# Performance work log

Measured on AMD Instinct MI355X. Metric: run time of the kernel, lower is better.

Reference implementation:

```python
import jax, jax.numpy as jnp
import numpy as np
from jax import lax

N_EXPERTS = 16
TOP_K = 2
D_MODEL = 512
D_FF = 2048


def setup_inputs() -> dict:
    key = jax.random.key(0)
    ks = jax.random.split(key, 7)
    s_in = 1.0 / np.sqrt(D_MODEL)
    s_ff = 1.0 / np.sqrt(D_FF)
    x = jax.random.normal(ks[0], (2, 2048, D_MODEL), dtype=jnp.float32)
    router_w = jax.random.uniform(ks[1], (N_EXPERTS, D_MODEL), jnp.float32, -s_in, s_in)
    router_b = jax.random.uniform(ks[2], (N_EXPERTS,), jnp.float32, -s_in, s_in)
    w1 = jax.random.uniform(ks[3], (N_EXPERTS, D_FF, D_MODEL), jnp.float32, -s_in, s_in)
    b1 = jax.random.uniform(ks[4], (N_EXPERTS, D_FF), jnp.float32, -s_in, s_in)
    w2 = jax.random.uniform(ks[5], (N_EXPERTS, D_MODEL, D_FF), jnp.float32, -s_ff, s_ff)
    b2 = jax.random.uniform(ks[6], (N_EXPERTS, D_MODEL), jnp.float32, -s_ff, s_ff)
    return {"x": x, "router_w": router_w, "router_b": router_b,
            "w1": w1, "b1": b1, "w2": w2, "b2": b2}


def reference(x, router_w, router_b, w1, b1, w2, b2):
    B, S, D = x.shape
    xt = x.reshape(-1, D)                                   # [T, D]
    logits = xt @ router_w.T + router_b                     # [T, E]
    probs = jax.nn.softmax(logits, axis=-1)
    topk_p, topk_i = lax.top_k(probs, TOP_K)                # [T, K]
    # Dense gate matrix: gate[t, e] = topk prob if expert e selected else 0.
    # Weighting by gate reproduces the masked gather/scatter-add exactly.
    onehot = jax.nn.one_hot(topk_i, N_EXPERTS, dtype=probs.dtype)  # [T, K, E]
    gates = jnp.sum(onehot * topk_p[..., None], axis=1)     # [T, E]

    def expert_step(acc, packed):
        w1e, b1e, w2e, b2e, ge = packed                     # per-expert params + gate col [T]
        h = jax.nn.gelu(xt @ w1e.T + b1e, approximate=False)  # [T, D_FF]
        y = h @ w2e.T + b2e                                 # [T, D]
        return acc + y * ge[:, None], None

    out, _ = lax.scan(expert_step, jnp.zeros_like(xt),
                      (w1, b1, w2, b2, gates.T))
    return out.reshape(B, S, D)
```

## Files before the change

kernel.cpp:

```cpp
#include <hip/hip_runtime.h>
#include <stdint.h>

#define T_TOK 4096
#define DM    512
#define DFF   2048
#define NE    16
#define NSLOT (T_TOK * 2)
#define NW    (16 * 2048 * 512)
#define MAXTILE 80
#define CONVB (2 * NW / 8 / 256)
#define ROUTB (T_TOK / 4)
#define KSPLIT 2

typedef __attribute__((ext_vector_type(8))) short  bf16x8;
typedef __attribute__((ext_vector_type(4))) float  f32x4;
typedef __attribute__((ext_vector_type(8))) unsigned short us8;

static __device__ __forceinline__ unsigned short f2bf(float f) {
    unsigned int u = __float_as_uint(f);
    u += 0x7FFFu + ((u >> 16) & 1u);
    return (unsigned short)(u >> 16);
}

static __device__ __forceinline__ void gload_lds16(const void* g, void* l) {
    __builtin_amdgcn_global_load_lds(
        (const __attribute__((address_space(1))) void*)g,
        (__attribute__((address_space(3))) void*)l, 16, 0, 0);
}

static __device__ __forceinline__ int xcd_chunk_logical(int bid, int total) {
    int k = bid & 7, seq = bid >> 3;
    int q = total >> 3, r = total & 7;
    int base = k * q + (k < r ? k : r);
    int len  = q + (k < r ? 1 : 0);
    return (seq < len) ? (base + seq) : total;
}

__global__ __launch_bounds__(256) void convert_router_kernel(
    const float* __restrict__ w1, const float* __restrict__ w2,
    unsigned short* __restrict__ w1b, unsigned short* __restrict__ w2b,
    const float* __restrict__ x, const float* __restrict__ rw,
    const float* __restrict__ rb, int* __restrict__ tok_e,
    float* __restrict__ tok_g, unsigned short* __restrict__ xb)
{
    __shared__ float rws[NE * DM];
    int tid = threadIdx.x;

    if (blockIdx.x >= ROUTB) {
        size_t i = ((size_t)(blockIdx.x - ROUTB) * 256 + tid) * 8;
        const float* src; unsigned short* dst;
        if (i < (size_t)NW) { src = w1 + i;        dst = w1b + i; }
        else                { src = w2 + (i - NW); dst = w2b + (i - NW); }
        f32x4 a = __builtin_nontemporal_load((const f32x4*)src);
        f32x4 b = __builtin_nontemporal_load((const f32x4*)(src + 4));
        us8 v;
        v[0] = f2bf(a.x); v[1] = f2bf(a.y); v[2] = f2bf(a.z); v[3] = f2bf(a.w);
        v[4] = f2bf(b.x); v[5] = f2bf(b.y); v[6] = f2bf(b.z); v[7] = f2bf(b.w);
        *(us8*)dst = v;
        return;
    }

    for (int i = 0; i < 8; ++i) {
        int idx = (tid + i * 256) * 4;
        *(f32x4*)&rws[idx] = *(const f32x4*)&rw[idx];
    }
    __syncthreads();

    int wid = tid >> 6, lane = tid & 63;
    int t = blockIdx.x * 4 + wid;

    float xv[8];
    const float* xp = x + (size_t)t * DM + lane * 8;
    *(f32x4*)&xv[0] = *(const f32x4*)xp;
    *(f32x4*)&xv[4] = *(const f32x4*)(xp + 4);

    us8 v;
    for (int i = 0; i < 8; ++i) v[i] = f2bf(xv[i]);
    *(us8*)&xb[(size_t)t * DM + lane * 8] = v;

    float acc[NE];
    for (int e = 0; e < NE; ++e) {
        const float* wp = &rws[e * DM + lane * 8];
        float a = 0.f;
        for (int i = 0; i < 8; ++i) a += xv[i] * wp[i];
        acc[e] = a;
    }
    for (int e = 0; e < NE; ++e) {
        float v2 = acc[e];
        for (int off = 32; off > 0; off >>= 1) v2 += __shfl_xor(v2, off);
        acc[e] = v2 + rb[e];
    }
    float m = acc[0];
    for (int e = 1; e < NE; ++e) m = fmaxf(m, acc[e]);
    float p[NE]; float s = 0.f;
    for (int e = 0; e < NE; ++e) { p[e] = expf(acc[e] - m); s += p[e]; }
    float inv = 1.f / s;
    int i0 = 0; float p0 = p[0];
    for (int e = 1; e < NE; ++e) if (p[e] > p0) { p0 = p[e]; i0 = e; }
    int i1 = (i0 == 0) ? 1 : 0; float p1 = p[i1];
    for (int e = 0; e < NE; ++e)
        if (e != i0 && p[e] > p1) { p1 = p[e]; i1 = e; }
    if (lane == 0) {
        tok_e[t * 2]     = i0;  tok_e[t * 2 + 1] = i1;
        tok_g[t * 2]     = p0 * inv;
        tok_g[t * 2 + 1] = p1 * inv;
    }
}

__global__ __launch_bounds__(1024) void compact_kernel(
    const int* __restrict__ tok_e, int* __restrict__ slot_token,
    int* __restrict__ tok_slot, int* __restrict__ eoff)
{
    __shared__ int wsum[16][NE];
    __shared__ int wbase[16][NE];
    __shared__ int ebl[NE];
    int tid = threadIdx.x;
    int wv = tid >> 6, lane = tid & 63;

    int ent[8];
    *(int4*)&ent[0] = *(const int4*)&tok_e[tid * 8];
    *(int4*)&ent[4] = *(const int4*)&tok_e[tid * 8 + 4];

    int cnt[NE], isc[NE];
#pragma unroll
    for (int e = 0; e < NE; ++e) {
        int c = 0;
#pragma unroll
        for (int i = 0; i < 8; ++i) c += (ent[i] == e) ? 1 : 0;
        int v = c;
#pragma unroll
        for (int off = 1; off < 64; off <<= 1) {
            int u = __shfl_up(v, off);
            if (lane >= off) v += u;
        }
        cnt[e] = c; isc[e] = v;
    }
    if (lane == 63) {
#pragma unroll
        for (int e = 0; e < NE; ++e) wsum[wv][e] = isc[e];
    }
    __syncthreads();
    if (wv == 0 && lane < NE) {
        int e = lane, s = 0;
#pragma unroll
        for (int w = 0; w < 16; ++w) { wbase[w][e] = s; s += wsum[w][e]; }
        int til = (s + 127) >> 7;
        int rs = s, rt = til;
#pragma unroll
        for (int off = 1; off < 16; off <<= 1) {
            int u1 = __shfl_up(rs, off);
            int u2 = __shfl_up(rt, off);
            if (lane >= off) { rs += u1; rt += u2; }
        }
        ebl[e] = rs - s;
        eoff[e] = rs - s;
        eoff[16 + e] = s;
        eoff[32 + e] = rt - til;
        if (e == NE - 1) eoff[48] = rt;
    }
    __syncthreads();
    int ofs[NE];
#pragma unroll
    for (int e = 0; e < NE; ++e)
        ofs[e] = ebl[e] + wbase[wv][e] + isc[e] - cnt[e];
#pragma unroll
    for (int i = 0; i < 8; ++i) {
        int ei = ent[i], s = 0;
#pragma unroll
        for (int e = 0; e < NE; ++e) if (ei == e) s = ofs[e];
        slot_token[s] = tid * 4 + (i >> 1);
        tok_slot[tid * 8 + i] = s;
#pragma unroll
        for (int e = 0; e < NE; ++e) if (ei == e) ofs[e] = s + 1;
    }
}

__global__ __launch_bounds__(256) void gemm1_kernel(
    const unsigned short* __restrict__ xb, const unsigned short* __restrict__ w1b,
    const float* __restrict__ b1, const int* __restrict__ slot_token,
    const int* __restrict__ eoff, unsigned short* __restrict__ h)
{
    __shared__ unsigned short smem[16384];
    __shared__ int tokrow[128];
    __shared__ int meta[49];
    unsigned short* As = smem;
    unsigned short* Bs = smem + 8192;

    int tid = threadIdx.x;
    if (tid < 49) meta[tid] = eoff[tid];
    __syncthreads();

    int lg = xcd_chunk_logical(blockIdx.x, meta[48] * 16);
    int slot_idx = lg >> 4;
    if (slot_idx >= meta[48]) return;
    int nB = (lg & 15) * 128;
    int e = 0;
    while (e < NE - 1 && meta[32 + e + 1] <= slot_idx) ++e;
    int mt  = slot_idx - meta[32 + e];
    int off = meta[e], cnt = meta[16 + e];
    int slot0 = off + mt * 128;
    int valid = cnt - mt * 128; if (valid > 128) valid = 128;

    if (tid < 128) {
        int s = slot0 + tid; if (s > NSLOT - 1) s = NSLOT - 1;
        tokrow[tid] = slot_token[s];
    }
    __syncthreads();

    f32x4 acc[16];
    for (int i = 0; i < 16; ++i) acc[i] = (f32x4){0.f, 0.f, 0.f, 0.f};

    const unsigned short* wb = w1b + ((size_t)e * DFF + nB) * DM;
    int wid = tid >> 6, l = tid & 63;
    int wm = (wid & 1) * 64, wn = (wid >> 1) * 64;
    int q = l >> 4, c = l & 15;

    for (int kt = 0; kt < DM / 64; ++kt) {
        for (int j = 0; j < 4; ++j) {
            int u = (wid * 4 + j) * 64 + l;
            int row = u >> 3, sc = (u & 7) ^ (row & 7);
            gload_lds16(xb + (size_t)tokrow[row] * DM + kt * 64 + sc * 8, &As[u * 8]);
        }
        for (int j = 0; j < 4; ++j) {
            int u = (wid * 4 + j) * 64 + l;
            int row = u >> 3, sc = (u & 7) ^ (row & 7);
            gload_lds16(wb + (size_t)row * DM + kt * 64 + sc * 8, &Bs[u * 8]);
        }
        __syncthreads();
        for (int ks = 0; ks < 2; ++ks) {
            int sw = ((ks * 4 + q) ^ (c & 7)) * 8;
            bf16x8 af[4], bv[4];
            for (int i = 0; i < 4; ++i) af[i] = *(bf16x8*)&As[(wm + i * 16 + c) * 64 + sw];
            for (int j = 0; j < 4; ++j) bv[j] = *(bf16x8*)&Bs[(wn + j * 16 + c) * 64 + sw];
            for (int i = 0; i < 4; ++i)
                for (int j = 0; j < 4; ++j)
                    acc[i * 4 + j] = __builtin_amdgcn_mfma_f32_16x16x32_bf16(
                        af[i], bv[j], acc[i * 4 + j], 0, 0, 0);
        }
        __syncthreads();
    }

    float bias[4];
    for (int j = 0; j < 4; ++j) bias[j] = b1[e * DFF + nB + wn + j * 16 + c];
    unsigned short* bounce = smem;
    for (int ph = 0; ph < 2; ++ph) {
        __syncthreads();
        if ((wid & 1) == ph) {
            for (int i = 0; i < 4; ++i)
                for (int j = 0; j < 4; ++j) {
                    f32x4 a = acc[i * 4 + j];
                    for (int r = 0; r < 4; ++r) {
                        int rl = i * 16 + q * 4 + r;
                        float z = a[r] + bias[j];
                        float u2 = z * fmaf(0.0356774081f, z * z, 0.7978845608f);
                        float ex = __expf(2.0f * u2);
                        float th = 1.0f - 2.0f * __builtin_amdgcn_rcpf(ex + 1.0f);
                        float g = 0.5f * z * (1.0f + th);
                        bounce[rl * 136 + wn + j * 16 + c] = f2bf(g);
                    }
                }
        }
        __syncthreads();
        for (int it = 0; it < 4; ++it) {
            int u2 = it * 256 + tid;
            int row = u2 >> 4, ch = u2 & 15;
            int gr = ph * 64 + row;
            if (gr < valid)
                *(us8*)&h[(size_t)(slot0 + gr) * DFF + nB + ch * 8] =
                    *(us8*)&bounce[row * 136 + ch * 8];
        }
    }
}

__global__ __launch_bounds__(256) void gemm2_kernel(
    const unsigned short* __restrict__ h, const unsigned short* __restrict__ w2b,
    const int* __restrict__ eoff, float* __restrict__ y)
{
    __shared__ unsigned short smem[16384];
    __shared__ int meta[49];
    unsigned short* As = smem;
    unsigned short* Bs = smem + 8192;

    int tid = threadIdx.x;
    if (tid < 49) meta[tid] = eoff[tid];
    __syncthreads();

    int lg = xcd_chunk_logical(blockIdx.x, meta[48] * 8);
    int slot_idx = lg >> 3;
    if (slot_idx >= meta[48]) return;
    int nB = (lg & 3) * 128;
    int z  = (lg >> 2) & 1;
    int e = 0;
    while (e < NE - 1 && meta[32 + e + 1] <= slot_idx) ++e;
    int mt  = slot_idx - meta[32 + e];
    int off = meta[e], cnt = meta[16 + e];
    int slot0 = off + mt * 128;
    int valid = cnt - mt * 128; if (valid > 128) valid = 128;

    f32x4 acc[16];
    for (int i = 0; i < 16; ++i) acc[i] = (f32x4){0.f, 0.f, 0.f, 0.f};

    const unsigned short* wb = w2b + ((size_t)e * DM + nB) * DFF
                             + (size_t)z * (DFF / KSPLIT);
    const unsigned short* hz = h + (size_t)z * (DFF / KSPLIT);
    int wid = tid >> 6, l = tid & 63;
    int wm = (wid & 1) * 64, wn = (wid >> 1) * 64;
    int q = l >> 4, c = l & 15;

    for (int kt = 0; kt < DFF / (64 * KSPLIT); ++kt) {
        for (int j = 0; j < 4; ++j) {
            int u = (wid * 4 + j) * 64 + l;
            int row = u >> 3, sc = (u & 7) ^ (row & 7);
            size_t s = slot0 + row; if (s > NSLOT - 1) s = NSLOT - 1;
            gload_lds16(hz + s * DFF + kt * 64 + sc * 8, &As[u * 8]);
        }
        for (int j = 0; j < 4; ++j) {
            int u = (wid * 4 + j) * 64 + l;
            int row = u >> 3, sc = (u & 7) ^ (row & 7);
            gload_lds16(wb + (size_t)row * DFF + kt * 64 + sc * 8, &Bs[u * 8]);
        }
        __syncthreads();
        for (int ks = 0; ks < 2; ++ks) {
            int sw = ((ks * 4 + q) ^ (c & 7)) * 8;
            bf16x8 af[4], bv[4];
            for (int i = 0; i < 4; ++i) af[i] = *(bf16x8*)&As[(wm + i * 16 + c) * 64 + sw];
            for (int j = 0; j < 4; ++j) bv[j] = *(bf16x8*)&Bs[(wn + j * 16 + c) * 64 + sw];
            for (int i = 0; i < 4; ++i)
                for (int j = 0; j < 4; ++j)
                    acc[i * 4 + j] = __builtin_amdgcn_mfma_f32_16x16x32_bf16(
                        af[i], bv[j], acc[i * 4 + j], 0, 0, 0);
        }
        __syncthreads();
    }

    float* yz = y + (size_t)z * NSLOT * DM;
    for (int i = 0; i < 4; ++i)
        for (int j = 0; j < 4; ++j) {
            int n = nB + wn + j * 16 + c;
            for (int r = 0; r < 4; ++r) {
                int rl = wm + i * 16 + q * 4 + r;
                if (rl < valid)
                    yz[(size_t)(slot0 + rl) * DM + n] = acc[i * 4 + j][r];
            }
        }
}

__global__ __launch_bounds__(256) void combine_kernel(
    const float* __restrict__ y, const float* __restrict__ b2,
    const int* __restrict__ tok_slot, const float* __restrict__ tok_g,
    const int* __restrict__ tok_e, float* __restrict__ out)
{
    int tid = threadIdx.x;
    int t = blockIdx.x * 2 + (tid >> 7);
    int d = (tid & 127) * 4;
    int s0 = tok_slot[t * 2], s1 = tok_slot[t * 2 + 1];
    float g0 = tok_g[t * 2], g1 = tok_g[t * 2 + 1];
    int e0 = tok_e[t * 2], e1 = tok_e[t * 2 + 1];
    const float* yB = y + (size_t)NSLOT * DM;
    f32x4 y0a = *(const f32x4*)&y [(size_t)s0 * DM + d];
    f32x4 y0b = *(const f32x4*)&yB[(size_t)s0 * DM + d];
    f32x4 y1a = *(const f32x4*)&y [(size_t)s1 * DM + d];
    f32x4 y1b = *(const f32x4*)&yB[(size_t)s1 * DM + d];
    f32x4 c0 = *(const f32x4*)&b2[e0 * DM + d];
    f32x4 c1 = *(const f32x4*)&b2[e1 * DM + d];
    f32x4 o;
    for (int i = 0; i < 4; ++i)
        o[i] = g0 * (y0a[i] + y0b[i] + c0[i]) + g1 * (y1a[i] + y1b[i] + c1[i]);
    *(f32x4*)&out[(size_t)t * DM + d] = o;
}

extern "C" void kernel_launch(void* const* d_in, const int* in_sizes, int n_in,
                              void* d_out, int out_size, void* d_ws, size_t ws_size,
                              hipStream_t stream) {
    const float* x  = (const float*)d_in[0];
    const float* rw = (const float*)d_in[1];
    const float* rb = (const float*)d_in[2];
    const float* w1 = (const float*)d_in[3];
    const float* b1 = (const float*)d_in[4];
    const float* w2 = (const float*)d_in[5];
    const float* b2 = (const float*)d_in[6];
    float* out = (float*)d_out;

    char* ws = (char*)d_ws;
    size_t o = 0;
    unsigned short* h   = (unsigned short*)(ws + o); o += (size_t)NSLOT * DFF * 2;
    unsigned short* w1b = (unsigned short*)(ws + o); o += (size_t)NW * 2;
    unsigned short* w2b = (unsigned short*)(ws + o); o += (size_t)NW * 2;
    unsigned short* xb  = (unsigned short*)(ws + o); o += (size_t)T_TOK * DM * 2;
    int*   tok_e      = (int*)(ws + o);   o += (size_t)NSLOT * 4;
    float* tok_g      = (float*)(ws + o); o += (size_t)NSLOT * 4;
    int*   tok_slot   = (int*)(ws + o);   o += (size_t)NSLOT * 4;
    int*   slot_token = (int*)(ws + o);   o += (size_t)NSLOT * 4;
    int*   eoff       = (int*)(ws + o);
    float* y = (float*)w1b;

    convert_router_kernel<<<ROUTB + CONVB, 256, 0, stream>>>(
        w1, w2, w1b, w2b, x, rw, rb, tok_e, tok_g, xb);
    compact_kernel<<<1, 1024, 0, stream>>>(
        tok_e, slot_token, tok_slot, eoff);
    gemm1_kernel<<<16 * MAXTILE, 256, 0, stream>>>(
        xb, w1b, b1, slot_token, eoff, h);
    gemm2_kernel<<<8 * MAXTILE, 256, 0, stream>>>(
        h, w2b, eoff, y);
    combine_kernel<<<T_TOK / 2, 256, 0, stream>>>(
        y, b2, tok_slot, tok_g, tok_e, out);
}
```

Before: 274.1 us.

## Double-buffer LDS tiles in both expert GEMMs and parallelize GELU epilogue

Both grouped GEMM kernels now keep two LDS stages. The global-to-LDS loads for the next K tile are issued before the MFMAs on the current tile, which removes the per-iteration barrier stall on load latency. The gemm1 epilogue now has all four waves convert half of their column fragments in each phase, using a narrower bounce buffer, instead of letting only half the waves work per phase. The cost is doubled shared memory per block (64KB), which lowers how many blocks fit on each CU.

New measurement: 270.7 us. About the same (-1.3%).

```diff
diff --git a/kernel.cpp b/kernel.cpp
--- a/kernel.cpp
+++ b/kernel.cpp
@@ -180,11 +180,9 @@
     const float* __restrict__ b1, const int* __restrict__ slot_token,
     const int* __restrict__ eoff, unsigned short* __restrict__ h)
 {
-    __shared__ unsigned short smem[16384];
+    __shared__ unsigned short smem[32768];
     __shared__ int tokrow[128];
     __shared__ int meta[49];
-    unsigned short* As = smem;
-    unsigned short* Bs = smem + 8192;
 
     int tid = threadIdx.x;
     if (tid < 49) meta[tid] = eoff[tid];
@@ -215,29 +213,40 @@
     int wm = (wid & 1) * 64, wn = (wid >> 1) * 64;
     int q = l >> 4, c = l & 15;
 
-    for (int kt = 0; kt < DM / 64; ++kt) {
+    auto stage = [&](int buf, int kt) {
+        unsigned short* A = &smem[buf * 16384];
+        unsigned short* B = A + 8192;
         for (int j = 0; j < 4; ++j) {
             int u = (wid * 4 + j) * 64 + l;
             int row = u >> 3, sc = (u & 7) ^ (row & 7);
-            gload_lds16(xb + (size_t)tokrow[row] * DM + kt * 64 + sc * 8, &As[u * 8]);
+            gload_lds16(xb + (size_t)tokrow[row] * DM + kt * 64 + sc * 8, &A[u * 8]);
         }
         for (int j = 0; j < 4; ++j) {
             int u = (wid * 4 + j) * 64 + l;
             int row = u >> 3, sc = (u & 7) ^ (row & 7);
-            gload_lds16(wb + (size_t)row * DM + kt * 64 + sc * 8, &Bs[u * 8]);
-        }
-        __syncthreads();
+            gload_lds16(wb + (size_t)row * DM + kt * 64 + sc * 8, &B[u * 8]);
+        }
+    };
+
+    stage(0, 0);
+    __syncthreads();
+    int cur = 0;
+    for (int kt = 0; kt < DM / 64; ++kt) {
+        if (kt + 1 < DM / 64) stage(cur ^ 1, kt + 1);
+        unsigned short* A = &smem[cur * 16384];
+        unsigned short* B = A + 8192;
         for (int ks = 0; ks < 2; ++ks) {
             int sw = ((ks * 4 + q) ^ (c & 7)) * 8;
             bf16x8 af[4], bv[4];
-            for (int i = 0; i < 4; ++i) af[i] = *(bf16x8*)&As[(wm + i * 16 + c) * 64 + sw];
-            for (int j = 0; j < 4; ++j) bv[j] = *(bf16x8*)&Bs[(wn + j * 16 + c) * 64 + sw];
+            for (int i = 0; i < 4; ++i) af[i] = *(bf16x8*)&A[(wm + i * 16 + c) * 64 + sw];
+            for (int j = 0; j < 4; ++j) bv[j] = *(bf16x8*)&B[(wn + j * 16 + c) * 64 + sw];
             for (int i = 0; i < 4; ++i)
                 for (int j = 0; j < 4; ++j)
                     acc[i * 4 + j] = __builtin_amdgcn_mfma_f32_16x16x32_bf16(
                         af[i], bv[j], acc[i * 4 + j], 0, 0, 0);
         }
         __syncthreads();
+        cur ^= 1;
     }
 
     float bias[4];
@@ -245,29 +254,30 @@
     unsigned short* bounce = smem;
     for (int ph = 0; ph < 2; ++ph) {
         __syncthreads();
-        if ((wid & 1) == ph) {
-            for (int i = 0; i < 4; ++i)
-                for (int j = 0; j < 4; ++j) {
-                    f32x4 a = acc[i * 4 + j];
-                    for (int r = 0; r < 4; ++r) {
-                        int rl = i * 16 + q * 4 + r;
-                        float z = a[r] + bias[j];
-                        float u2 = z * fmaf(0.0356774081f, z * z, 0.7978845608f);
-                        float ex = __expf(2.0f * u2);
-                        float th = 1.0f - 2.0f * __builtin_amdgcn_rcpf(ex + 1.0f);
-                        float g = 0.5f * z * (1.0f + th);
-                        bounce[rl * 136 + wn + j * 16 + c] = f2bf(g);
-                    }
+        for (int jj = 0; jj < 2; ++jj) {
+            int j = 2 * ph + jj;
+            for (int i = 0; i < 4; ++i) {
+                f32x4 a = acc[i * 4 + j];
+                for (int r = 0; r < 4; ++r) {
+                    int rl = wm + i * 16 + q * 4 + r;
+                    float z = a[r] + bias[j];
+                    float u2 = z * fmaf(0.0356774081f, z * z, 0.7978845608f);
+                    float ex = __expf(2.0f * u2);
+                    float th = 1.0f - 2.0f * __builtin_amdgcn_rcpf(ex + 1.0f);
+                    float g = 0.5f * z * (1.0f + th);
+                    bounce[rl * 80 + (wn >> 1) + jj * 16 + c] = f2bf(g);
                 }
+            }
         }
         __syncthreads();
         for (int it = 0; it < 4; ++it) {
             int u2 = it * 256 + tid;
-            int row = u2 >> 4, ch = u2 & 15;
-            int gr = ph * 64 + row;
-            if (gr < valid)
-                *(us8*)&h[(size_t)(slot0 + gr) * DFF + nB + ch * 8] =
-                    *(us8*)&bounce[row * 136 + ch * 8];
+            int row = u2 >> 3, ch = u2 & 7;
+            int cl = ch * 8;
+            int n  = (cl < 32 ? cl : 32 + cl) + 32 * ph;
+            if (row < valid)
+                *(us8*)&h[(size_t)(slot0 + row) * DFF + nB + n] =
+                    *(us8*)&bounce[row * 80 + cl];
         }
     }
 }
@@ -276,10 +286,8 @@
     const unsigned short* __restrict__ h, const unsigned short* __restrict__ w2b,
     const int* __restrict__ eoff, float* __restrict__ y)
 {
-    __shared__ unsigned short smem[16384];
+    __shared__ unsigned short smem[32768];
     __shared__ int meta[49];
-    unsigned short* As = smem;
-    unsigned short* Bs = smem + 8192;
 
     int tid = threadIdx.x;
     if (tid < 49) meta[tid] = eoff[tid];
@@ -307,30 +315,42 @@
     int wm = (wid & 1) * 64, wn = (wid >> 1) * 64;
     int q = l >> 4, c = l & 15;
 
-    for (int kt = 0; kt < DFF / (64 * KSPLIT); ++kt) {
+    auto stage = [&](int buf, int kt) {
+        unsigned short* A = &smem[buf * 16384];
+        unsigned short* B = A + 8192;
         for (int j = 0; j < 4; ++j) {
             int u = (wid * 4 + j) * 64 + l;
             int row = u >> 3, sc = (u & 7) ^ (row & 7);
             size_t s = slot0 + row; if (s > NSLOT - 1) s = NSLOT - 1;
-            gload_lds16(hz + s * DFF + kt * 64 + sc * 8, &As[u * 8]);
+            gload_lds16(hz + s * DFF + kt * 64 + sc * 8, &A[u * 8]);
         }
         for (int j = 0; j < 4; ++j) {
             int u = (wid * 4 + j) * 64 + l;
             int row = u >> 3, sc = (u & 7) ^ (row & 7);
-            gload_lds16(wb + (size_t)row * DFF + kt * 64 + sc * 8, &Bs[u * 8]);
-        }
-        __syncthreads();
+            gload_lds16(wb + (size_t)row * DFF + kt * 64 + sc * 8, &B[u * 8]);
+        }
+    };
+
+    const int NT = DFF / (64 * KSPLIT);
+    stage(0, 0);
+    __syncthreads();
+    int cur = 0;
+    for (int kt = 0; kt < NT; ++kt) {
+        if (kt + 1 < NT) stage(cur ^ 1, kt + 1);
+        unsigned short* A = &smem[cur * 16384];
+        unsigned short* B = A + 8192;
         for (int ks = 0; ks < 2; ++ks) {
             int sw = ((ks * 4 + q) ^ (c & 7)) * 8;
             bf16x8 af[4], bv[4];
-            for (int i = 0; i < 4; ++i) af[i] = *(bf16x8*)&As[(wm + i * 16 + c) * 64 + sw];
-            for (int j = 0; j < 4; ++j) bv[j] = *(bf16x8*)&Bs[(wn + j * 16 + c) * 64 + sw];
+            for (int i = 0; i < 4; ++i) af[i] = *(bf16x8*)&A[(wm + i * 16 + c) * 64 + sw];
+            for (int j = 0; j < 4; ++j) bv[j] = *(bf16x8*)&B[(wn + j * 16 + c) * 64 + sw];
             for (int i = 0; i < 4; ++i)
                 for (int j = 0; j < 4; ++j)
                     acc[i * 4 + j] = __builtin_amdgcn_mfma_f32_16x16x32_bf16(
                         af[i], bv[j], acc[i * 4 + j], 0, 0, 0);
         }
         __syncthreads();
+        cur ^= 1;
     }
 
     float* yz = y + (size_t)z * NSLOT * DM;
```
